# Optimization experiments

Measured on AMD Instinct MI355X. Metric: run time of the kernel, lower is better.

Reference implementation:

```python
import jax, jax.numpy as jnp
import numpy as np
from jax import lax

C = 512          # n_embed
M = 512          # num_memory_slots
K = 3            # conv_kernel_size
B, T = 8, 8192
EPS = 1e-5


def _layernorm(x, g, b):
    mu = jnp.mean(x, axis=-1, keepdims=True)
    var = jnp.var(x, axis=-1, keepdims=True)
    return (x - mu) * lax.rsqrt(var + EPS) * g + b


def setup_inputs() -> dict:
    key = jax.random.key(0)
    ks = jax.random.split(key, 10)
    s = 0.02
    return {
        "x": jax.random.normal(ks[0], (B, T, C), jnp.float32),
        "conv_w": jax.random.normal(ks[1], (C, 1, K), jnp.float32) * s,   # depthwise (O, I/g=1, K)
        "conv_b": jnp.zeros((C,), jnp.float32),
        "memory_bank": jax.random.normal(ks[2], (M, C), jnp.float32) * (1.0 / np.sqrt(C)),
        "gate_w": jax.random.normal(ks[3], (C, 2 * C), jnp.float32) * s,
        "gate_b": jnp.zeros((2 * C,), jnp.float32),
        "w1": jax.random.normal(ks[4], (C, 4 * C), jnp.float32) * s,
        "b1": jnp.zeros((4 * C,), jnp.float32),
        "w2": jax.random.normal(ks[5], (4 * C, C), jnp.float32) * s,
        "b2": jnp.zeros((C,), jnp.float32),
        "ln1_g": jnp.ones((C,), jnp.float32),
        "ln1_b": jnp.zeros((C,), jnp.float32),
        "ln2_g": jnp.ones((C,), jnp.float32),
        "ln2_b": jnp.zeros((C,), jnp.float32),
    }


def reference(x, conv_w, conv_b, memory_bank, gate_w, gate_b,
              w1, b1, w2, b2, ln1_g, ln1_b, ln2_g, ln2_b):
    residual = x
    x_norm = _layernorm(x, ln1_g, ln1_b)                      # (B,T,C)

    # causal depthwise conv: left-pad by K-1 (PyTorch pads both sides then slices [:T])
    xt = jnp.transpose(x_norm, (0, 2, 1))                     # (B,C,T)
    local = lax.conv_general_dilated(
        xt, conv_w, window_strides=(1,), padding=[(K - 1, 0)],
        dimension_numbers=("NCT", "OIT", "NCT"), feature_group_count=C)
    local = jnp.transpose(local + conv_b[None, :, None], (0, 2, 1))  # (B,T,C)

    # memory-bank softmax attention
    scores = jnp.einsum("btc,mc->btm", x_norm, memory_bank)   # (B,T,M)
    weights = jax.nn.softmax(scores, axis=-1)
    global_ctx = jnp.einsum("btm,mc->btc", weights, memory_bank)

    # sigmoid gating
    gates = x_norm @ gate_w + gate_b                          # (B,T,2C)
    lg, gg = gates[..., :C], gates[..., C:]
    fused = jax.nn.sigmoid(lg) * local + jax.nn.sigmoid(gg) * global_ctx

    x = residual + fused
    h = _layernorm(x, ln2_g, ln2_b)
    ffn = jax.nn.gelu(h @ w1 + b1, approximate=False) @ w2 + b2  # dropout is identity (eval)
    return x + ffn
```

## Files before the change

kernel.cpp:

```cpp
#include <hip/hip_runtime.h>
#include <math.h>

#define NTOK 65536
#define T_   8192
#define C_   512

typedef short short8 __attribute__((ext_vector_type(8)));
typedef float f32x4  __attribute__((ext_vector_type(4)));

#define GLDS(gp, lp) __builtin_amdgcn_global_load_lds( \
    (__attribute__((address_space(1))) void*)(void*)(gp), \
    (__attribute__((address_space(3))) void*)(lp), 16, 0, 0)

__device__ __forceinline__ unsigned short f2bf(float f){
  unsigned x = __float_as_uint(f);
  x += 0x7fffu + ((x >> 16) & 1u);
  return (unsigned short)(x >> 16);
}
__device__ __forceinline__ float bflo(unsigned p){ return __uint_as_float(p << 16); }
__device__ __forceinline__ float bfhi(unsigned p){ return __uint_as_float(p & 0xffff0000u); }
__device__ __forceinline__ float bfs(unsigned short u){ return __uint_as_float(((unsigned)u) << 16); }
__device__ __forceinline__ unsigned pack2(float a, float b){
  return (unsigned)f2bf(a) | ((unsigned)f2bf(b) << 16);
}
__device__ __forceinline__ int xcd_remap(int flat, int nwg){
  int q = nwg >> 3, r = nwg & 7;
  int xcd = flat & 7, idx = flat >> 3;
  return (xcd < r ? xcd * (q + 1) : r * (q + 1) + (xcd - r) * q) + idx;
}

__global__ __launch_bounds__(256) void k_convert(const float* __restrict__ src,
                                                 unsigned short* __restrict__ dst, int n){
  int i = blockIdx.x * 256 + threadIdx.x;
  if (i < n) dst[i] = f2bf(src[i]);
}
__global__ __launch_bounds__(256) void k_transpose_t(const float* __restrict__ src,
                                                     unsigned short* __restrict__ dst,
                                                     int R, int S){
  __shared__ float tile[64][65];
  int ntS = S >> 6;
  int tr = blockIdx.x / ntS, ts = blockIdx.x - tr * ntS;
  int tx = threadIdx.x & 63, tg = threadIdx.x >> 6;
  #pragma unroll
  for (int rr = tg; rr < 64; rr += 4)
    tile[rr][tx] = src[(size_t)(tr * 64 + rr) * S + ts * 64 + tx];
  __syncthreads();
  #pragma unroll
  for (int rr = tg; rr < 64; rr += 4)
    dst[(size_t)(ts * 64 + rr) * R + tr * 64 + tx] = f2bf(tile[tx][rr]);
}

__global__ __launch_bounds__(256) void k_ln(const float* __restrict__ x,
                                            const float* __restrict__ g,
                                            const float* __restrict__ b,
                                            unsigned* __restrict__ outbf){
  int row = blockIdx.x;
  int t = threadIdx.x;
  float2 v = ((const float2*)(x + (size_t)row * C_))[t];
  float s = v.x + v.y, ss = v.x * v.x + v.y * v.y;
  #pragma unroll
  for (int o = 32; o; o >>= 1){ s += __shfl_down(s, o); ss += __shfl_down(ss, o); }
  __shared__ float red[8];
  if ((t & 63) == 0){ red[t >> 6] = s; red[4 + (t >> 6)] = ss; }
  __syncthreads();
  float S = red[0] + red[1] + red[2] + red[3];
  float Q = red[4] + red[5] + red[6] + red[7];
  float mu  = S * (1.0f / C_);
  float var = Q * (1.0f / C_) - mu * mu;
  float rs = rsqrtf(var + 1e-5f);
  float y0 = (v.x - mu) * rs * g[2*t]   + b[2*t];
  float y1 = (v.y - mu) * rs * g[2*t+1] + b[2*t+1];
  outbf[(size_t)row * 256 + t] = pack2(y0, y1);
}

__global__ __launch_bounds__(256) void k_conv(const unsigned* __restrict__ xn,
                                              const float* __restrict__ w,
                                              const float* __restrict__ bias,
                                              unsigned* __restrict__ loc,
                                              int base){
  size_t idx = (size_t)blockIdx.x * 256 + threadIdx.x;
  size_t n = (idx >> 8) + (size_t)base;
  int cp = (int)(idx & 255);
  int t = (int)(n & (T_ - 1));
  unsigned v0 = xn[n * 256 + cp];
  unsigned v1 = (t >= 1) ? xn[(n - 1) * 256 + cp] : 0u;
  unsigned v2 = (t >= 2) ? xn[(n - 2) * 256 + cp] : 0u;
  int c = cp * 2;
  float r0 = bias[c]     + bflo(v0)*w[c*3+2] + bflo(v1)*w[c*3+1] + bflo(v2)*w[c*3+0];
  float r1 = bias[c + 1] + bfhi(v0)*w[c*3+5] + bfhi(v1)*w[c*3+4] + bfhi(v2)*w[c*3+3];
  loc[idx] = pack2(r0, r1);
}

__global__ __launch_bounds__(256) void k_softmax_ip(unsigned* __restrict__ sw){
  int row = blockIdx.x;
  int t = threadIdx.x;
  unsigned p = sw[(size_t)row * 256 + t];
  float vx = bflo(p), vy = bfhi(p);
  float mx = fmaxf(vx, vy);
  #pragma unroll
  for (int o = 32; o; o >>= 1) mx = fmaxf(mx, __shfl_xor(mx, o));
  __shared__ float red[8];
  int w = t >> 6;
  if ((t & 63) == 0) red[w] = mx;
  __syncthreads();
  mx = fmaxf(fmaxf(red[0], red[1]), fmaxf(red[2], red[3]));
  float e0 = __expf(vx - mx), e1 = __expf(vy - mx);
  float s = e0 + e1;
  #pragma unroll
  for (int o = 32; o; o >>= 1) s += __shfl_xor(s, o);
  if ((t & 63) == 0) red[4 + w] = s;
  __syncthreads();
  float inv = 1.0f / (red[4] + red[5] + red[6] + red[7]);
  sw[(size_t)row * 256 + t] = pack2(e0 * inv, e1 * inv);
}

#define PH_PRE  { __builtin_amdgcn_s_barrier(); \
                  asm volatile("s_waitcnt lgkmcnt(0)" ::: "memory"); \
                  __builtin_amdgcn_sched_barrier(0); }
#define PH_END  __builtin_amdgcn_s_barrier();
#define VMW2    asm volatile("s_waitcnt vmcnt(2)" ::: "memory");
#define VMW0    asm volatile("s_waitcnt vmcnt(0)" ::: "memory");

template<int EPI, int K, int N>
__global__ __launch_bounds__(512, 2) void k_g256(const unsigned short* __restrict__ A,
                                                 const unsigned short* __restrict__ Bt,
                                                 void* __restrict__ out,
                                                 const float* __restrict__ bias,
                                                 const float* __restrict__ add){
  __shared__ char smem[131072];
  const int tid  = threadIdx.x;
  const int lane = tid & 63;
  const int w    = tid >> 6;
  const int wr   = w >> 2, wc = w & 3;
  const int nwg  = gridDim.x * gridDim.y;
  const int wgid = xcd_remap(blockIdx.y * gridDim.x + blockIdx.x, nwg);
  const long bcol = (long)(wgid % gridDim.x) * 256;
  const long brow = (long)(wgid / gridDim.x) * 256;
  const int lr = lane & 15;
  const int lk = (lane >> 4) * 16;
  const int srow  = tid >> 3;
  const int sbyte = ((tid & 7) * 16) ^ ((srow & 7) << 4);
  const unsigned swb = (unsigned)(w * 1024);
  const int rsw = (lr & 7) << 4;

  f32x4 acc[8][4];
  #pragma unroll
  for (int i = 0; i < 8; i++)
    #pragma unroll
    for (int j = 0; j < 4; j++){ f32x4 z = {0.f,0.f,0.f,0.f}; acc[i][j] = z; }

  const char* Ab = (const char*)(A + brow * (long)K);
  const char* Bb = (const char*)(Bt + bcol * (long)K);

  auto ST = [&](const char* g, int ldsoff, int row0, int kt){
    GLDS(g + ((long)(row0 + srow) * K + (long)kt * 64) * 2 + sbyte,
         smem + ldsoff + row0 * 128 + swb);
  };
  auto stA0 = [&](int b, int kt){ ST(Ab, b*32768, 0,  kt); ST(Ab, b*32768, 128, kt); };
  auto stA1 = [&](int b, int kt){ ST(Ab, b*32768, 64, kt); ST(Ab, b*32768, 192, kt); };
  auto stB0 = [&](int b, int kt){ ST(Bb, 65536+b*32768, 0,   kt); ST(Bb, 65536+b*32768, 64,  kt); };
  auto stB1 = [&](int b, int kt){ ST(Bb, 65536+b*32768, 128, kt); ST(Bb, 65536+b*32768, 192, kt); };

  short8 afr[4][2], bfr[2][2];
  auto RDA = [&](int b, int qm){
    #pragma unroll
    for (int mj = 0; mj < 4; mj++)
      #pragma unroll
      for (int kk = 0; kk < 2; kk++)
        afr[mj][kk] = *(const short8*)(smem + b*32768 +
            (wr*128 + (qm*4+mj)*16 + lr) * 128 + ((kk*64 + lk) ^ rsw));
  };
  auto RDB = [&](int b, int qn){
    #pragma unroll
    for (int nj = 0; nj < 2; nj++)
      #pragma unroll
      for (int kk = 0; kk < 2; kk++)
        bfr[nj][kk] = *(const short8*)(smem + 65536 + b*32768 +
            (wc*64 + (qn*2+nj)*16 + lr) * 128 + ((kk*64 + lk) ^ rsw));
  };
  auto MM = [&](int qm, int qn){
    __builtin_amdgcn_s_setprio(1);
    #pragma unroll
    for (int mj = 0; mj < 4; mj++)
      #pragma unroll
      for (int nj = 0; nj < 2; nj++)
        #pragma unroll
        for (int kk = 0; kk < 2; kk++)
          acc[qm*4+mj][qn*2+nj] =
            __builtin_amdgcn_mfma_f32_16x16x32_bf16(afr[mj][kk], bfr[nj][kk],
                                                    acc[qm*4+mj][qn*2+nj], 0, 0, 0);
    __builtin_amdgcn_s_setprio(0);
  };

  constexpr int nt    = K >> 6;
  constexpr int niter = nt >> 1;

  stA0(0, 0); stA1(0, 0); stB0(0, 0); stB1(0, 0);
  stA0(1, 1);
  VMW2;
  __builtin_amdgcn_s_barrier();

  #pragma unroll 1
  for (int i = 0; i < niter; i++){
    const int t = 2 * i;
    RDA(0,0); RDB(0,0); stA1(1, t+1);
    PH_PRE; MM(0,0); PH_END;
    RDA(0,1); stB0(1, t+1);
    PH_PRE; MM(1,0); PH_END;
    RDA(0,0); RDB(0,1); stB1(1, t+1);
    PH_PRE; MM(0,1); PH_END;
    RDA(0,1); if (t + 2 < nt) stA0(0, t+2);
    PH_PRE; MM(1,1);
    if (t + 2 < nt) { VMW2; } else { VMW0; }
    PH_END;
    RDA(1,0); RDB(1,0); if (t + 2 < nt) stA1(0, t+2);
    PH_PRE; MM(0,0); PH_END;
    RDA(1,1); if (t + 2 < nt) stB0(0, t+2);
    PH_PRE; MM(1,0); PH_END;
    RDA(1,0); RDB(1,1); if (t + 2 < nt) stB1(0, t+2);
    PH_PRE; MM(0,1); PH_END;
    RDA(1,1); if (t + 3 < nt) stA0(1, t+3);
    PH_PRE; MM(1,1);
    if (i + 1 < niter){ if (t + 3 < nt) { VMW2; } else { VMW0; } }
    PH_END;
  }

  const long rb = brow + wr * 128;
  const long cb = bcol + wc * 64;
  #pragma unroll
  for (int mi = 0; mi < 8; mi++){
    #pragma unroll
    for (int ni = 0; ni < 4; ni++){
      long rg0 = rb + mi * 16 + (lane >> 4) * 4;
      long cg  = cb + ni * 16 + lr;
      #pragma unroll
      for (int j = 0; j < 4; j++){
        long oi = (rg0 + j) * (long)N + cg;
        float v = acc[mi][ni][j];
        if (EPI == 1){
          ((unsigned short*)out)[oi] = f2bf(v);
        } else if (EPI == 3){
          v += bias[cg];
          v = 0.5f * v * (1.0f + erff(v * 0.70710678118654752f));
          ((unsigned short*)out)[oi] = f2bf(v);
        } else {
          v += bias[cg] + add[oi];
          ((float*)out)[oi] = v;
        }
      }
    }
  }
}

__global__ __launch_bounds__(512, 2) void k_gc256(const unsigned short* __restrict__ A,
                                                  const unsigned short* __restrict__ Bt,
                                                  const float* __restrict__ gb,
                                                  const unsigned short* __restrict__ loc,
                                                  const unsigned short* __restrict__ ctx,
                                                  const float* __restrict__ x,
                                                  float* __restrict__ x2){
  __shared__ char smem[131072];
  const int tid  = threadIdx.x;
  const int lane = tid & 63;
  const int w    = tid >> 6;
  const int wr   = w >> 2, wc = w & 3;
  const int nwg  = gridDim.x * gridDim.y;
  const int wgid = xcd_remap(blockIdx.y * gridDim.x + blockIdx.x, nwg);
  const int  bcol = (wgid % gridDim.x) * 128;
  const long brow = (long)(wgid / gridDim.x) * 256;
  const int K = 512;
  const int lr = lane & 15;
  const int lk = (lane >> 4) * 16;
  const int srow  = tid >> 3;
  const int sbyte = ((tid & 7) * 16) ^ ((srow & 7) << 4);
  const unsigned swb = (unsigned)(w * 1024);
  const int rsw = (lr & 7) << 4;

  f32x4 acc[8][2][2];
  #pragma unroll
  for (int i = 0; i < 8; i++)
    #pragma unroll
    for (int j = 0; j < 2; j++)
      #pragma unroll
      for (int h = 0; h < 2; h++){ f32x4 z = {0.f,0.f,0.f,0.f}; acc[i][j][h] = z; }

  const char* Ab  = (const char*)(A + brow * (long)K);
  const char* BbL = (const char*)(Bt + (long)bcol * K);
  const char* BbG = (const char*)(Bt + (long)(512 + bcol) * K);

  auto ST = [&](const char* g, int ldsoff, int row0, int kt){
    GLDS(g + ((long)(row0 + srow) * K + (long)kt * 64) * 2 + sbyte,
         smem + ldsoff + row0 * 128 + swb);
  };
  auto stA0 = [&](int b, int kt){ ST(Ab, b*32768, 0,  kt); ST(Ab, b*32768, 128, kt); };
  auto stA1 = [&](int b, int kt){ ST(Ab, b*32768, 64, kt); ST(Ab, b*32768, 192, kt); };
  auto stBL = [&](int b, int kt){ ST(BbL, 65536+b*32768,       0, kt); ST(BbL, 65536+b*32768,       64, kt); };
  auto stBG = [&](int b, int kt){ ST(BbG, 65536+b*32768+16384, 0, kt); ST(BbG, 65536+b*32768+16384, 64, kt); };

  short8 afr[4][2], bfr[2][2];
  auto RDA = [&](int b, int qm){
    #pragma unroll
    for (int mj = 0; mj < 4; mj++)
      #pragma unroll
      for (int kk = 0; kk < 2; kk++)
        afr[mj][kk] = *(const short8*)(smem + b*32768 +
            (wr*128 + (qm*4+mj)*16 + lr) * 128 + ((kk*64 + lk) ^ rsw));
  };
  auto RDB = [&](int b, int h){
    #pragma unroll
    for (int nj = 0; nj < 2; nj++)
      #pragma unroll
      for (int kk = 0; kk < 2; kk++)
        bfr[nj][kk] = *(const short8*)(smem + 65536 + b*32768 + h*16384 +
            (wc*32 + nj*16 + lr) * 128 + ((kk*64 + lk) ^ rsw));
  };
  auto MM = [&](int qm, int h){
    __builtin_amdgcn_s_setprio(1);
    #pragma unroll
    for (int mj = 0; mj < 4; mj++)
      #pragma unroll
      for (int nj = 0; nj < 2; nj++)
        #pragma unroll
        for (int kk = 0; kk < 2; kk++)
          acc[qm*4+mj][nj][h] =
            __builtin_amdgcn_mfma_f32_16x16x32_bf16(afr[mj][kk], bfr[nj][kk],
                                                    acc[qm*4+mj][nj][h], 0, 0, 0);
    __builtin_amdgcn_s_setprio(0);
  };

  constexpr int nt = 8, niter = 4;

  stA0(0, 0); stA1(0, 0); stBL(0, 0); stBG(0, 0);
  stA0(1, 1);
  VMW2;
  __builtin_amdgcn_s_barrier();

  #pragma unroll 1
  for (int i = 0; i < niter; i++){
    const int t = 2 * i;
    RDA(0,0); RDB(0,0); stA1(1, t+1);
    PH_PRE; MM(0,0); PH_END;
    RDA(0,1); stBL(1, t+1);
    PH_PRE; MM(1,0); PH_END;
    RDA(0,0); RDB(0,1); stBG(1, t+1);
    PH_PRE; MM(0,1); PH_END;
    RDA(0,1); if (t + 2 < nt) stA0(0, t+2);
    PH_PRE; MM(1,1);
    if (t + 2 < nt) { VMW2; } else { VMW0; }
    PH_END;
    RDA(1,0); RDB(1,0); if (t + 2 < nt) stA1(0, t+2);
    PH_PRE; MM(0,0); PH_END;
    RDA(1,1); if (t + 2 < nt) stBL(0, t+2);
    PH_PRE; MM(1,0); PH_END;
    RDA(1,0); RDB(1,1); if (t + 2 < nt) stBG(0, t+2);
    PH_PRE; MM(0,1); PH_END;
    RDA(1,1); if (t + 3 < nt) stA0(1, t+3);
    PH_PRE; MM(1,1);
    if (i + 1 < niter){ if (t + 3 < nt) { VMW2; } else { VMW0; } }
    PH_END;
  }

  const long rbase = brow + wr * 128;
  const int  cb_   = bcol + wc * 32;
  #pragma unroll
  for (int mi = 0; mi < 8; mi++){
    #pragma unroll
    for (int ni = 0; ni < 2; ni++){
      long rg0 = rbase + mi * 16 + (lane >> 4) * 4;
      int  cg  = cb_ + ni * 16 + lr;
      float bL = gb[cg], bG = gb[512 + cg];
      #pragma unroll
      for (int j = 0; j < 4; j++){
        long rg = rg0 + j;
        long oi = rg * 512 + cg;
        float vL = 1.0f / (1.0f + __expf(-(acc[mi][ni][0][j] + bL)));
        float vG = 1.0f / (1.0f + __expf(-(acc[mi][ni][1][j] + bG)));
        x2[oi] = x[oi] + vL * bfs(loc[oi]) + vG * bfs(ctx[oi]);
      }
    }
  }
}

extern "C" void kernel_launch(void* const* d_in, const int* in_sizes, int n_in,
                              void* d_out, int out_size, void* d_ws, size_t ws_size,
                              hipStream_t stream){
  const float* x      = (const float*)d_in[0];
  const float* conv_w = (const float*)d_in[1];
  const float* conv_b = (const float*)d_in[2];
  const float* mb     = (const float*)d_in[3];
  const float* gate_w = (const float*)d_in[4];
  const float* gate_b = (const float*)d_in[5];
  const float* w1     = (const float*)d_in[6];
  const float* b1     = (const float*)d_in[7];
  const float* w2     = (const float*)d_in[8];
  const float* b2     = (const float*)d_in[9];
  const float* ln1g   = (const float*)d_in[10];
  const float* ln1b   = (const float*)d_in[11];
  const float* ln2g   = (const float*)d_in[12];
  const float* ln2b   = (const float*)d_in[13];

  char* ws = (char*)d_ws;
  const size_t MB = 1024ull * 1024ull;
  unsigned short* mb_bf = (unsigned short*)(ws + 0);
  unsigned short* mbT   = (unsigned short*)(ws + 512 * 1024);
  unsigned short* gwT   = (unsigned short*)(ws + 1 * MB);
  unsigned short* w1T   = (unsigned short*)(ws + 2 * MB);
  unsigned short* w2T   = (unsigned short*)(ws + 4 * MB);
  unsigned short* xn    = (unsigned short*)(ws + 8 * MB);
  char* region = ws + 72 * MB;

  int S;
  if      (ws_size >= 264 * MB) S = 65536;
  else if (ws_size >= 120 * MB) S = 16384;
  else                          S = 4096;
  const int S2 = S / 2;
  const int NC  = NTOK / S;
  const int NC2 = NTOK / S2;

  unsigned short* loc_c = (unsigned short*)(region);
  unsigned short* ctx_c = (unsigned short*)(region + (size_t)S * 1024);
  unsigned short* sco_c = (unsigned short*)(region + (size_t)S * 2048);
  unsigned short* f1    = (unsigned short*)(region);

  k_convert    <<<1024, 256, 0, stream>>>(mb, mb_bf, 512 * 512);
  k_transpose_t<<<  64, 256, 0, stream>>>(mb, mbT, 512, 512);
  k_transpose_t<<< 128, 256, 0, stream>>>(gate_w, gwT, 512, 1024);
  k_transpose_t<<< 256, 256, 0, stream>>>(w1, w1T, 512, 2048);
  k_transpose_t<<< 256, 256, 0, stream>>>(w2, w2T, 2048, 512);

  k_ln<<<NTOK, 256, 0, stream>>>(x, ln1g, ln1b, (unsigned*)xn);

  for (int c = 0; c < NC; c++){
    const int base = c * S;
    const unsigned short* xnc = xn + (size_t)base * 512;
    k_conv<<<S, 256, 0, stream>>>((const unsigned*)xn, conv_w, conv_b,
                                  (unsigned*)loc_c, base);
    k_g256<1, 512, 512><<<dim3(2, S / 256), 512, 0, stream>>>(xnc, mb_bf, sco_c,
                                                              nullptr, nullptr);
    k_softmax_ip<<<S, 256, 0, stream>>>((unsigned*)sco_c);
    k_g256<1, 512, 512><<<dim3(2, S / 256), 512, 0, stream>>>(sco_c, mbT, ctx_c,
                                                              nullptr, nullptr);
    k_gc256<<<dim3(4, S / 256), 512, 0, stream>>>(xnc, gwT, gate_b,
                                                  loc_c, ctx_c,
                                                  x + (size_t)base * 512,
                                                  (float*)d_out + (size_t)base * 512);
  }

  k_ln<<<NTOK, 256, 0, stream>>>((const float*)d_out, ln2g, ln2b, (unsigned*)xn);

  for (int c = 0; c < NC2; c++){
    const int base = c * S2;
    k_g256<3, 512, 2048><<<dim3(8, S2 / 256), 512, 0, stream>>>(xn + (size_t)base * 512,
                                                                w1T, f1, b1, nullptr);
    k_g256<4, 2048, 512><<<dim3(2, S2 / 256), 512, 0, stream>>>(f1, w2T,
                                                                (float*)d_out + (size_t)base * 512,
                                                                b2,
                                                                (const float*)d_out + (size_t)base * 512);
  }
}
```

Measured before the change: 900.1 us.

## Shrink GEMM tiles to 128x128 with simple double-buffered pipeline

Replaces the 256x256-tile GEMM and gated-GEMM kernels with 128-row tiles (128x128 for the plain GEMM, 128x64 for the gated one) that use half the LDS and launch bounds allowing four blocks per CU. The multi-phase interleaved load/compute schedule becomes a plain double buffer that waits for all outstanding loads each k-step. The aim is more resident waves and more blocks to fill the GPU, at the cost of lower data reuse per tile and less overlap of memory loads with MFMA work.

```diff
diff --git a/kernel.cpp b/kernel.cpp
--- a/kernel.cpp
+++ b/kernel.cpp
@@ -118,24 +118,24 @@
                   asm volatile("s_waitcnt lgkmcnt(0)" ::: "memory"); \
                   __builtin_amdgcn_sched_barrier(0); }
 #define PH_END  __builtin_amdgcn_s_barrier();
-#define VMW2    asm volatile("s_waitcnt vmcnt(2)" ::: "memory");
 #define VMW0    asm volatile("s_waitcnt vmcnt(0)" ::: "memory");
 
 template<int EPI, int K, int N>
-__global__ __launch_bounds__(512, 2) void k_g256(const unsigned short* __restrict__ A,
+__global__ __launch_bounds__(512, 4) void k_g128(const unsigned short* __restrict__ A,
                                                  const unsigned short* __restrict__ Bt,
                                                  void* __restrict__ out,
                                                  const float* __restrict__ bias,
                                                  const float* __restrict__ add){
-  __shared__ char smem[131072];
+  __shared__ char smem[65536];
   const int tid  = threadIdx.x;
   const int lane = tid & 63;
   const int w    = tid >> 6;
   const int wr   = w >> 2, wc = w & 3;
-  const int nwg  = gridDim.x * gridDim.y;
-  const int wgid = xcd_remap(blockIdx.y * gridDim.x + blockIdx.x, nwg);
-  const long bcol = (long)(wgid % gridDim.x) * 256;
-  const long brow = (long)(wgid / gridDim.x) * 256;
+  const int gx   = gridDim.x;
+  const int nwg  = gx * gridDim.y;
+  const int wgid = xcd_remap(blockIdx.y * gx + blockIdx.x, nwg);
+  const long bcol = (long)(wgid % gx) * 128;
+  const long brow = (long)(wgid / gx) * 128;
   const int lr = lane & 15;
   const int lk = (lane >> 4) * 16;
   const int srow  = tid >> 3;
@@ -143,11 +143,11 @@
   const unsigned swb = (unsigned)(w * 1024);
   const int rsw = (lr & 7) << 4;
 
-  f32x4 acc[8][4];
-  #pragma unroll
-  for (int i = 0; i < 8; i++)
-    #pragma unroll
-    for (int j = 0; j < 4; j++){ f32x4 z = {0.f,0.f,0.f,0.f}; acc[i][j] = z; }
+  f32x4 acc[4][2];
+  #pragma unroll
+  for (int i = 0; i < 4; i++)
+    #pragma unroll
+    for (int j = 0; j < 2; j++){ f32x4 z = {0.f,0.f,0.f,0.f}; acc[i][j] = z; }
 
   const char* Ab = (const char*)(A + brow * (long)K);
   const char* Bb = (const char*)(Bt + bcol * (long)K);
@@ -156,81 +156,59 @@
     GLDS(g + ((long)(row0 + srow) * K + (long)kt * 64) * 2 + sbyte,
          smem + ldsoff + row0 * 128 + swb);
   };
-  auto stA0 = [&](int b, int kt){ ST(Ab, b*32768, 0,  kt); ST(Ab, b*32768, 128, kt); };
-  auto stA1 = [&](int b, int kt){ ST(Ab, b*32768, 64, kt); ST(Ab, b*32768, 192, kt); };
-  auto stB0 = [&](int b, int kt){ ST(Bb, 65536+b*32768, 0,   kt); ST(Bb, 65536+b*32768, 64,  kt); };
-  auto stB1 = [&](int b, int kt){ ST(Bb, 65536+b*32768, 128, kt); ST(Bb, 65536+b*32768, 192, kt); };
+  auto stA = [&](int b, int kt){ ST(Ab, b*16384, 0, kt); ST(Ab, b*16384, 64, kt); };
+  auto stB = [&](int b, int kt){ ST(Bb, 32768+b*16384, 0, kt); ST(Bb, 32768+b*16384, 64, kt); };
 
   short8 afr[4][2], bfr[2][2];
-  auto RDA = [&](int b, int qm){
-    #pragma unroll
-    for (int mj = 0; mj < 4; mj++)
+  auto RD = [&](int b){
+    #pragma unroll
+    for (int mi = 0; mi < 4; mi++)
       #pragma unroll
       for (int kk = 0; kk < 2; kk++)
-        afr[mj][kk] = *(const short8*)(smem + b*32768 +
-            (wr*128 + (qm*4+mj)*16 + lr) * 128 + ((kk*64 + lk) ^ rsw));
-  };
-  auto RDB = [&](int b, int qn){
-    #pragma unroll
-    for (int nj = 0; nj < 2; nj++)
+        afr[mi][kk] = *(const short8*)(smem + b*16384 +
+            (wr*64 + mi*16 + lr) * 128 + ((kk*64 + lk) ^ rsw));
+    #pragma unroll
+    for (int ni = 0; ni < 2; ni++)
       #pragma unroll
       for (int kk = 0; kk < 2; kk++)
-        bfr[nj][kk] = *(const short8*)(smem + 65536 + b*32768 +
-            (wc*64 + (qn*2+nj)*16 + lr) * 128 + ((kk*64 + lk) ^ rsw));
-  };
-  auto MM = [&](int qm, int qn){
+        bfr[ni][kk] = *(const short8*)(smem + 32768 + b*16384 +
+            (wc*32 + ni*16 + lr) * 128 + ((kk*64 + lk) ^ rsw));
+  };
+  auto MM = [&](){
     __builtin_amdgcn_s_setprio(1);
     #pragma unroll
-    for (int mj = 0; mj < 4; mj++)
-      #pragma unroll
-      for (int nj = 0; nj < 2; nj++)
+    for (int mi = 0; mi < 4; mi++)
+      #pragma unroll
+      for (int ni = 0; ni < 2; ni++)
         #pragma unroll
         for (int kk = 0; kk < 2; kk++)
-          acc[qm*4+mj][qn*2+nj] =
-            __builtin_amdgcn_mfma_f32_16x16x32_bf16(afr[mj][kk], bfr[nj][kk],
-                                                    acc[qm*4+mj][qn*2+nj], 0, 0, 0);
+          acc[mi][ni] = __builtin_amdgcn_mfma_f32_16x16x32_bf16(afr[mi][kk], bfr[ni][kk],
+                                                                acc[mi][ni], 0, 0, 0);
     __builtin_amdgcn_s_setprio(0);
   };
 
-  constexpr int nt    = K >> 6;
-  constexpr int niter = nt >> 1;
-
-  stA0(0, 0); stA1(0, 0); stB0(0, 0); stB1(0, 0);
-  stA0(1, 1);
-  VMW2;
+  constexpr int nt = K >> 6;
+
+  stA(0, 0); stB(0, 0);
+  VMW0;
   __builtin_amdgcn_s_barrier();
 
   #pragma unroll 1
-  for (int i = 0; i < niter; i++){
-    const int t = 2 * i;
-    RDA(0,0); RDB(0,0); stA1(1, t+1);
-    PH_PRE; MM(0,0); PH_END;
-    RDA(0,1); stB0(1, t+1);
-    PH_PRE; MM(1,0); PH_END;
-    RDA(0,0); RDB(0,1); stB1(1, t+1);
-    PH_PRE; MM(0,1); PH_END;
-    RDA(0,1); if (t + 2 < nt) stA0(0, t+2);
-    PH_PRE; MM(1,1);
-    if (t + 2 < nt) { VMW2; } else { VMW0; }
+  for (int t = 0; t < nt; t++){
+    const int b = t & 1;
+    RD(b);
+    if (t + 1 < nt){ stA(b ^ 1, t + 1); stB(b ^ 1, t + 1); }
+    PH_PRE; MM();
+    if (t + 1 < nt) { VMW0; }
     PH_END;
-    RDA(1,0); RDB(1,0); if (t + 2 < nt) stA1(0, t+2);
-    PH_PRE; MM(0,0); PH_END;
-    RDA(1,1); if (t + 2 < nt) stB0(0, t+2);
-    PH_PRE; MM(1,0); PH_END;
-    RDA(1,0); RDB(1,1); if (t + 2 < nt) stB1(0, t+2);
-    PH_PRE; MM(0,1); PH_END;
-    RDA(1,1); if (t + 3 < nt) stA0(1, t+3);
-    PH_PRE; MM(1,1);
-    if (i + 1 < niter){ if (t + 3 < nt) { VMW2; } else { VMW0; } }
-    PH_END;
-  }
-
-  const long rb = brow + wr * 128;
-  const long cb = bcol + wc * 64;
-  #pragma unroll
-  for (int mi = 0; mi < 8; mi++){
-    #pragma unroll
-    for (int ni = 0; ni < 4; ni++){
+  }
+
+  const long rb = brow + wr * 64;
+  const long cb = bcol + wc * 32;
+  #pragma unroll
+  for (int mi = 0; mi < 4; mi++){
+    #pragma unroll
+    for (int ni = 0; ni < 2; ni++){
       long rg0 = rb + mi * 16 + (lane >> 4) * 4;
       long cg  = cb + ni * 16 + lr;
       #pragma unroll
@@ -252,22 +230,23 @@
   }
 }
 
-__global__ __launch_bounds__(512, 2) void k_gc256(const unsigned short* __restrict__ A,
+__global__ __launch_bounds__(512, 4) void k_gc128(const unsigned short* __restrict__ A,
                                                   const unsigned short* __restrict__ Bt,
                                                   const float* __restrict__ gb,
                                                   const unsigned short* __restrict__ loc,
                                                   const unsigned short* __restrict__ ctx,
                                                   const float* __restrict__ x,
                                                   float* __restrict__ x2){
-  __shared__ char smem[131072];
+  __shared__ char smem[65536];
   const int tid  = threadIdx.x;
   const int lane = tid & 63;
   const int w    = tid >> 6;
-  const int wr   = w >> 2, wc = w & 3;
-  const int nwg  = gridDim.x * gridDim.y;
-  const int wgid = xcd_remap(blockIdx.y * gridDim.x + blockIdx.x, nwg);
-  const int  bcol = (wgid % gridDim.x) * 128;
-  const long brow = (long)(wgid / gridDim.x) * 256;
+  const int wr   = w >> 1, wc = w & 1;
+  const int gx   = gridDim.x;
+  const int nwg  = gx * gridDim.y;
+  const int wgid = xcd_remap(blockIdx.y * gx + blockIdx.x, nwg);
+  const int  bcol = (wgid % gx) * 64;
+  const long brow = (long)(wgid / gx) * 128;
   const int K = 512;
   const int lr = lane & 15;
   const int lk = (lane >> 4) * 16;
@@ -276,9 +255,9 @@
   const unsigned swb = (unsigned)(w * 1024);
   const int rsw = (lr & 7) << 4;
 
-  f32x4 acc[8][2][2];
-  #pragma unroll
-  for (int i = 0; i < 8; i++)
+  f32x4 acc[2][2][2];
+  #pragma unroll
+  for (int i = 0; i < 2; i++)
     #pragma unroll
     for (int j = 0; j < 2; j++)
       #pragma unroll
@@ -292,82 +271,67 @@
     GLDS(g + ((long)(row0 + srow) * K + (long)kt * 64) * 2 + sbyte,
          smem + ldsoff + row0 * 128 + swb);
   };
-  auto stA0 = [&](int b, int kt){ ST(Ab, b*32768, 0,  kt); ST(Ab, b*32768, 128, kt); };
-  auto stA1 = [&](int b, int kt){ ST(Ab, b*32768, 64, kt); ST(Ab, b*32768, 192, kt); };
-  auto stBL = [&](int b, int kt){ ST(BbL, 65536+b*32768,       0, kt); ST(BbL, 65536+b*32768,       64, kt); };
-  auto stBG = [&](int b, int kt){ ST(BbG, 65536+b*32768+16384, 0, kt); ST(BbG, 65536+b*32768+16384, 64, kt); };
-
-  short8 afr[4][2], bfr[2][2];
-  auto RDA = [&](int b, int qm){
-    #pragma unroll
-    for (int mj = 0; mj < 4; mj++)
+  auto stA = [&](int b, int kt){ ST(Ab, b*16384, 0, kt); ST(Ab, b*16384, 64, kt); };
+  auto stB = [&](int b, int kt){ ST(BbL, 32768+b*8192, 0, kt); ST(BbG, 49152+b*8192, 0, kt); };
+
+  short8 afr[2][2], blf[2][2], bgf[2][2];
+  auto RD = [&](int b){
+    #pragma unroll
+    for (int mi = 0; mi < 2; mi++)
       #pragma unroll
       for (int kk = 0; kk < 2; kk++)
-        afr[mj][kk] = *(const short8*)(smem + b*32768 +
-            (wr*128 + (qm*4+mj)*16 + lr) * 128 + ((kk*64 + lk) ^ rsw));
-  };
-  auto RDB = [&](int b, int h){
-    #pragma unroll
-    for (int nj = 0; nj < 2; nj++)
-      #pragma unroll
-      for (int kk = 0; kk < 2; kk++)
-        bfr[nj][kk] = *(const short8*)(smem + 65536 + b*32768 + h*16384 +
-            (wc*32 + nj*16 + lr) * 128 + ((kk*64 + lk) ^ rsw));
-  };
-  auto MM = [&](int qm, int h){
+        afr[mi][kk] = *(const short8*)(smem + b*16384 +
+            (wr*32 + mi*16 + lr) * 128 + ((kk*64 + lk) ^ rsw));
+    #pragma unroll
+    for (int ni = 0; ni < 2; ni++)
+      #pragma unroll
+      for (int kk = 0; kk < 2; kk++){
+        blf[ni][kk] = *(const short8*)(smem + 32768 + b*8192 +
+            (wc*32 + ni*16 + lr) * 128 + ((kk*64 + lk) ^ rsw));
+        bgf[ni][kk] = *(const short8*)(smem + 49152 + b*8192 +
+            (wc*32 + ni*16 + lr) * 128 + ((kk*64 + lk) ^ rsw));
+      }
+  };
+  auto MM = [&](){
     __builtin_amdgcn_s_setprio(1);
     #pragma unroll
-    for (int mj = 0; mj < 4; mj++)
-      #pragma unroll
-      for (int nj = 0; nj < 2; nj++)
+    for (int mi = 0; mi < 2; mi++)
+      #pragma unroll
+      for (int ni = 0; ni < 2; ni++)
         #pragma unroll
-        for (int kk = 0; kk < 2; kk++)
-          acc[qm*4+mj][nj][h] =
-            __builtin_amdgcn_mfma_f32_16x16x32_bf16(afr[mj][kk], bfr[nj][kk],
-                                                    acc[qm*4+mj][nj][h], 0, 0, 0);
+        for (int kk = 0; kk < 2; kk++){
+          acc[mi][ni][0] = __builtin_amdgcn_mfma_f32_16x16x32_bf16(afr[mi][kk], blf[ni][kk],
+                                                                   acc[mi][ni][0], 0, 0, 0);
+          acc[mi][ni][1] = __builtin_amdgcn_mfma_f32_16x16x32_bf16(afr[mi][kk], bgf[ni][kk],
+                                                                   acc[mi][ni][1], 0, 0, 0);
+        }
     __builtin_amdgcn_s_setprio(0);
   };
 
-  constexpr int nt = 8, niter = 4;
-
-  stA0(0, 0); stA1(0, 0); stBL(0, 0); stBG(0, 0);
-  stA0(1, 1);
-  VMW2;
+  constexpr int nt = 8;
+
+  stA(0, 0); stB(0, 0);
+  VMW0;
   __builtin_amdgcn_s_barrier();
 
   #pragma unroll 1
-  for (int i = 0; i < niter; i++){
-    const int t = 2 * i;
-    RDA(0,0); RDB(0,0); stA1(1, t+1);
-    PH_PRE; MM(0,0); PH_END;
-    RDA(0,1); stBL(1, t+1);
-    PH_PRE; MM(1,0); PH_END;
-    RDA(0,0); RDB(0,1); stBG(1, t+1);
-    PH_PRE; MM(0,1); PH_END;
-    RDA(0,1); if (t + 2 < nt) stA0(0, t+2);
-    PH_PRE; MM(1,1);
-    if (t + 2 < nt) { VMW2; } else { VMW0; }
+  for (int t = 0; t < nt; t++){
+    const int b = t & 1;
+    RD(b);
+    if (t + 1 < nt){ stA(b ^ 1, t + 1); stB(b ^ 1, t + 1); }
+    PH_PRE; MM();
+    if (t + 1 < nt) { VMW0; }
     PH_END;
-    RDA(1,0); RDB(1,0); if (t + 2 < nt) stA1(0, t+2);
-    PH_PRE; MM(0,0); PH_END;
-    RDA(1,1); if (t + 2 < nt) stBL(0, t+2);
-    PH_PRE; MM(1,0); PH_END;
-    RDA(1,0); RDB(1,1); if (t + 2 < nt) stBG(0, t+2);
-    PH_PRE; MM(0,1); PH_END;
-    RDA(1,1); if (t + 3 < nt) stA0(1, t+3);
-    PH_PRE; MM(1,1);
-    if (i + 1 < niter){ if (t + 3 < nt) { VMW2; } else { VMW0; } }
-    PH_END;
-  }
-
-  const long rbase = brow + wr * 128;
-  const int  cb_   = bcol + wc * 32;
-  #pragma unroll
-  for (int mi = 0; mi < 8; mi++){
+  }
+
+  const long rb = brow + wr * 32;
+  const int  cb = bcol + wc * 32;
+  #pragma unroll
+  for (int mi = 0; mi < 2; mi++){
     #pragma unroll
     for (int ni = 0; ni < 2; ni++){
-      long rg0 = rbase + mi * 16 + (lane >> 4) * 4;
-      int  cg  = cb_ + ni * 16 + lr;
+      long rg0 = rb + mi * 16 + (lane >> 4) * 4;
+      int  cg  = cb + ni * 16 + lr;
       float bL = gb[cg], bG = gb[512 + cg];
       #pragma unroll
       for (int j = 0; j < 4; j++){
@@ -435,12 +399,12 @@
     const unsigned short* xnc = xn + (size_t)base * 512;
     k_conv<<<S, 256, 0, stream>>>((const unsigned*)xn, conv_w, conv_b,
                                   (unsigned*)loc_c, base);
-    k_g256<1, 512, 512><<<dim3(2, S / 256), 512, 0, stream>>>(xnc, mb_bf, sco_c,
+    k_g128<1, 512, 512><<<dim3(4, S / 128), 512, 0, stream>>>(xnc, mb_bf, sco_c,
                                                               nullptr, nullptr);
     k_softmax_ip<<<S, 256, 0, stream>>>((unsigned*)sco_c);
-    k_g256<1, 512, 512><<<dim3(2, S / 256), 512, 0, stream>>>(sco_c, mbT, ctx_c,
+    k_g128<1, 512, 512><<<dim3(4, S / 128), 512, 0, stream>>>(sco_c, mbT, ctx_c,
                                                               nullptr, nullptr);
-    k_gc256<<<dim3(4, S / 256), 512, 0, stream>>>(xnc, gwT, gate_b,
+    k_gc128<<<dim3(8, S / 128), 512, 0, stream>>>(xnc, gwT, gate_b,
                                                   loc_c, ctx_c,
                                                   x + (size_t)base * 512,
                                                   (float*)d_out + (size_t)base * 512);
@@ -450,9 +414,9 @@
 
   for (int c = 0; c < NC2; c++){
     const int base = c * S2;
-    k_g256<3, 512, 2048><<<dim3(8, S2 / 256), 512, 0, stream>>>(xn + (size_t)base * 512,
-                                                                w1T, f1, b1, nullptr);
-    k_g256<4, 2048, 512><<<dim3(2, S2 / 256), 512, 0, stream>>>(f1, w2T,
+    k_g128<3, 512, 2048><<<dim3(16, S2 / 128), 512, 0, stream>>>(xn + (size_t)base * 512,
+                                                                 w1T, f1, b1, nullptr);
+    k_g128<4, 2048, 512><<<dim3(4, S2 / 128), 512, 0, stream>>>(f1, w2T,
                                                                 (float*)d_out + (size_t)base * 512,
                                                                 b2,
                                                                 (const float*)d_out + (size_t)base * 512);
```

Measured after the change: 926.8 us. +3.0%, slower.
